# Optimization experiments

Measured on AMD Instinct MI355X. Metric: run time of the kernel, lower is better.

## Reference

```python
import jax, jax.numpy as jnp
import numpy as np

D_MODEL = 1024
N_HEADS = 16
HEAD_DIM = D_MODEL // N_HEADS
D_FF = 4 * D_MODEL
SEQ = 2048
BATCH = 2
EPS = 1e-6


def setup_inputs() -> dict:
    key = jax.random.key(0)
    ks = jax.random.split(key, 8)
    s = 0.02
    return {
        "x": jax.random.normal(ks[0], (SEQ, BATCH, D_MODEL), dtype=jnp.float32),
        "g1": jnp.ones((D_MODEL,), dtype=jnp.float32),                # norm1 weight
        "g2": jnp.ones((D_MODEL,), dtype=jnp.float32),                # norm2 weight
        "Wq": jax.random.normal(ks[1], (N_HEADS, D_MODEL, HEAD_DIM), dtype=jnp.float32) * s,
        "Wk": jax.random.normal(ks[2], (N_HEADS, D_MODEL, HEAD_DIM), dtype=jnp.float32) * s,
        "Wv": jax.random.normal(ks[3], (N_HEADS, D_MODEL, HEAD_DIM), dtype=jnp.float32) * s,
        "Wo": jax.random.normal(ks[4], (D_MODEL, D_MODEL), dtype=jnp.float32) * s,
        "W1": jax.random.normal(ks[5], (D_MODEL, D_FF), dtype=jnp.float32) * s,
        "W2": jax.random.normal(ks[6], (D_FF, D_MODEL), dtype=jnp.float32) * s,
    }


def _rmsnorm(x, g):
    rms = jnp.sqrt(jnp.mean(x * x, axis=-1, keepdims=True) + EPS)
    return g * (x / rms)


def _block(x, g1, g2, Wq, Wk, Wv, Wo, W1, W2):
    S = x.shape[0]
    scale = HEAD_DIM ** -0.5
    # --- attention (pre-norm) ---
    h = _rmsnorm(x, g1)                              # (S, B, D)
    Q = jnp.einsum('sbd,hdk->bhsk', h, Wq)           # (B, H, S, K)
    K = jnp.einsum('sbd,hdk->bhsk', h, Wk)
    V = jnp.einsum('sbd,hdk->bhsk', h, Wv)
    scores = jnp.einsum('bhsk,bhtk->bhst', Q, K) * scale
    causal = jnp.tril(jnp.ones((S, S), dtype=bool))
    scores = jnp.where(causal, scores, -jnp.inf)
    attn = jax.nn.softmax(scores, axis=-1)
    ctx = jnp.einsum('bhst,bhtk->sbhk', attn, V)     # heads concatenated in order
    ctx = ctx.reshape(S, x.shape[1], D_MODEL)
    x = x + ctx @ Wo
    # --- FFN (pre-norm) ---
    h2 = _rmsnorm(x, g2)
    x = x + jax.nn.silu(h2 @ W1) @ W2
    return x


def reference(x, g1, g2, Wq, Wk, Wv, Wo, W1, W2):
    return _block(x, g1, g2, Wq, Wk, Wv, Wo, W1, W2)
```

## Files before the change

kernel.cpp:

```cpp
#include <hip/hip_runtime.h>

typedef unsigned short u16;
typedef __bf16 bf16x8 __attribute__((ext_vector_type(8)));
typedef u16 u16x8 __attribute__((ext_vector_type(8)));
typedef u16 u16x4 __attribute__((ext_vector_type(4)));
typedef float f32x4 __attribute__((ext_vector_type(4)));

__device__ __forceinline__ u16 f2bf(float f) {
    union { float f; unsigned int u; } x; x.f = f;
    unsigned int r = x.u + 0x7FFFu + ((x.u >> 16) & 1u);
    return (u16)(r >> 16);
}

__device__ __forceinline__ u16 f2bf_hw(float f) {
    union { __bf16 b; u16 u; } x; x.b = (__bf16)f; return x.u;
}

__device__ __forceinline__ void gload_lds16(const u16* g, u16* l) {
    __builtin_amdgcn_global_load_lds(
        (const __attribute__((address_space(1))) unsigned int*)g,
        (__attribute__((address_space(3))) unsigned int*)l, 16, 0, 0);
}


__global__ __launch_bounds__(256) void qkvT_k(
    const float* __restrict__ Wq, const float* __restrict__ Wk,
    const float* __restrict__ Wv, u16* __restrict__ out)
{
    __shared__ float T[64][65];
    const int d0 = blockIdx.x * 64;
    const int y = blockIdx.y;
    const int wsel = y >> 4, h = y & 15;
    const float* W = (wsel == 0) ? Wq : (wsel == 1) ? Wk : Wv;
    const float scale = (wsel == 0) ? 0.125f * 1.44269504088896f : 1.0f;
    const int tid = threadIdx.x;
    const int tr = tid >> 4;
    const int tc = (tid & 15) * 4;
    #pragma unroll
    for (int k = 0; k < 4; k++) {
        f32x4 v = *(const f32x4*)(W + (size_t)h * 65536 + (size_t)(d0 + 16 * k + tr) * 64 + tc);
        T[16 * k + tr][tc]     = v[0];
        T[16 * k + tr][tc + 1] = v[1];
        T[16 * k + tr][tc + 2] = v[2];
        T[16 * k + tr][tc + 3] = v[3];
    }
    __syncthreads();
    #pragma unroll
    for (int k = 0; k < 4; k++) {
        const int kk = 16 * k + tr;
        u16x4 o;
        #pragma unroll
        for (int i = 0; i < 4; i++) o[i] = f2bf(T[tc + i][kk] * scale);
        *(u16x4*)(out + (size_t)(wsel * 1024 + h * 64 + kk) * 1024 + d0 + tc) = o;
    }
}

__global__ __launch_bounds__(256) void transT_k(
    const float* __restrict__ in, u16* __restrict__ out, int R, int C)
{
    __shared__ float T[64][65];
    const int r0 = blockIdx.x * 64, c0 = blockIdx.y * 64;
    const int tid = threadIdx.x;
    const int tr = tid >> 4;
    const int tc = (tid & 15) * 4;
    #pragma unroll
    for (int k = 0; k < 4; k++) {
        f32x4 v = *(const f32x4*)(in + (size_t)(c0 + 16 * k + tr) * R + r0 + tc);
        T[16 * k + tr][tc]     = v[0];
        T[16 * k + tr][tc + 1] = v[1];
        T[16 * k + tr][tc + 2] = v[2];
        T[16 * k + tr][tc + 3] = v[3];
    }
    __syncthreads();
    #pragma unroll
    for (int k = 0; k < 4; k++) {
        const int rl = 16 * k + tr;
        u16x4 o;
        #pragma unroll
        for (int i = 0; i < 4; i++) o[i] = f2bf(T[tc + i][rl]);
        *(u16x4*)(out + (size_t)(r0 + rl) * C + c0 + tc) = o;
    }
}

__global__ __launch_bounds__(256) void vtrans_k(const u16* __restrict__ qkv, u16* __restrict__ vT)
{
    __shared__ u16 T[64][72];
    const int bh = blockIdx.x, b = bh >> 4, h = bh & 15;
    const int s0 = blockIdx.y * 64;
    const int tid = threadIdx.x;
    const int r = tid >> 2, c0 = (tid & 3) * 16;
    const u16* src = qkv + ((size_t)((s0 + r) * 2 + b)) * 3072 + 2048 + h * 64 + c0;
    *(u16x8*)&T[r][c0] = *(const u16x8*)src;
    *(u16x8*)&T[r][c0 + 8] = *(const u16x8*)(src + 8);
    __syncthreads();
    u16x8 o0, o1;
    #pragma unroll
    for (int i = 0; i < 8; i++) o0[i] = T[c0 + i][r];
    #pragma unroll
    for (int i = 0; i < 8; i++) o1[i] = T[c0 + 8 + i][r];
    u16* dst = vT + (size_t)(bh * 64 + r) * 2048 + s0 + c0;
    *(u16x8*)dst = o0;
    *(u16x8*)(dst + 8) = o1;
}

__global__ __launch_bounds__(256) void rmsnorm_k(
    const float* __restrict__ x, const float* __restrict__ g, u16* __restrict__ out)
{
    const int row = blockIdx.x;
    const int tid = threadIdx.x;
    const float* xr = x + (size_t)row * 1024;
    f32x4 v = *(const f32x4*)(xr + tid * 4);
    float ss = v[0] * v[0] + v[1] * v[1] + v[2] * v[2] + v[3] * v[3];
    #pragma unroll
    for (int off = 32; off > 0; off >>= 1) ss += __shfl_down(ss, off);
    __shared__ float red[4];
    if ((tid & 63) == 0) red[tid >> 6] = ss;
    __syncthreads();
    float sum = red[0] + red[1] + red[2] + red[3];
    float rinv = rsqrtf(sum * (1.0f / 1024.0f) + 1e-6f);
    f32x4 gv = *(const f32x4*)(g + tid * 4);
    u16x4 o;
    #pragma unroll
    for (int i = 0; i < 4; i++) o[i] = f2bf(v[i] * gv[i] * rinv);
    *(u16x4*)(out + (size_t)row * 1024 + tid * 4) = o;
}

__global__ __launch_bounds__(256) void addred_norm_k(
    const float* __restrict__ res, const float* __restrict__ p0,
    const float* __restrict__ p1, const float* __restrict__ g,
    float* __restrict__ xout, u16* __restrict__ hout)
{
    const int row = blockIdx.x;
    const int tid = threadIdx.x;
    const size_t base = (size_t)row * 1024 + tid * 4;
    f32x4 a = *(const f32x4*)(res + base);
    f32x4 b = *(const f32x4*)(p0 + base);
    f32x4 c = *(const f32x4*)(p1 + base);
    f32x4 o = a + b + c;
    *(f32x4*)(xout + base) = o;
    float ss = o[0] * o[0] + o[1] * o[1] + o[2] * o[2] + o[3] * o[3];
    #pragma unroll
    for (int off = 32; off > 0; off >>= 1) ss += __shfl_down(ss, off);
    __shared__ float red[4];
    if ((tid & 63) == 0) red[tid >> 6] = ss;
    __syncthreads();
    float sum = red[0] + red[1] + red[2] + red[3];
    float rinv = rsqrtf(sum * (1.0f / 1024.0f) + 1e-6f);
    f32x4 gv = *(const f32x4*)(g + tid * 4);
    u16x4 hv;
    #pragma unroll
    for (int i = 0; i < 4; i++) hv[i] = f2bf(o[i] * gv[i] * rinv);
    *(u16x4*)(hout + base) = hv;
}

__global__ __launch_bounds__(256) void addred4_k(
    const float* __restrict__ xm, const float* __restrict__ a0,
    const float* __restrict__ a1, const float* __restrict__ a2,
    const float* __restrict__ a3, float* __restrict__ out)
{
    int i = (blockIdx.x * 256 + threadIdx.x) * 4;
    f32x4 v = *(const f32x4*)(xm + i);
    v = v + *(const f32x4*)(a0 + i);
    v = v + *(const f32x4*)(a1 + i);
    v = v + *(const f32x4*)(a2 + i);
    v = v + *(const f32x4*)(a3 + i);
    *(f32x4*)(out + i) = v;
}

template <int MODE>
__global__ __launch_bounds__(256) void gemm_bt_k(
    const u16* __restrict__ A, const u16* __restrict__ BT,
    u16* __restrict__ outB, float* __restrict__ outF, const float* __restrict__ res,
    int M, int N, int K, int klen)
{
    __shared__ u16 As[2][128 * 64];
    __shared__ u16 Bs[2][128 * 64];
    const int tid = threadIdx.x;
    const int lane = tid & 63, w = tid >> 6;
    const int wm = w >> 1, wn = w & 1;
    const int quad = lane >> 4, l15 = lane & 15;
    const int bid = blockIdx.x + gridDim.x * blockIdx.y;
    const int bj = bid >> 3;
    const int m0 = ((bid & 7) * 4 + (bj & 3)) * 128;
    const int n0 = (bj >> 2) * 128;
    const int kbeg = blockIdx.z * klen;

    f32x4 acc[4][4] = {};

    const int srow = (w << 3) + (lane >> 3);
    const int swz = ((lane & 7) ^ (lane >> 3)) << 3;
    const u16* aA = A + (size_t)(m0 + srow) * K + kbeg + swz;
    const u16* aB = BT + (size_t)(n0 + srow) * K + kbeg + swz;
    const int wo = w * 512;
    const int rsw = (l15 & 7) << 3;

    #pragma unroll
    for (int c = 0; c < 4; c++) {
        gload_lds16(aA + (size_t)(c * 32) * K, &As[0][0] + c * 2048 + wo);
        gload_lds16(aB + (size_t)(c * 32) * K, &Bs[0][0] + c * 2048 + wo);
    }

    int cur = 0;
    for (int k0 = 0; k0 < klen; k0 += 64) {
        __syncthreads();
        if (k0 + 64 < klen) {
            #pragma unroll
            for (int c = 0; c < 4; c++) {
                gload_lds16(aA + (size_t)(c * 32) * K + k0 + 64, &As[cur ^ 1][0] + c * 2048 + wo);
                gload_lds16(aB + (size_t)(c * 32) * K + k0 + 64, &Bs[cur ^ 1][0] + c * 2048 + wo);
            }
        }
        const u16* AB = &As[cur][0];
        const u16* BB = &Bs[cur][0];
        #pragma unroll
        for (int kh = 0; kh < 2; kh++) {
            const int cb = ((kh * 4 + quad) << 3);
            bf16x8 af[4], bfr[4];
            #pragma unroll
            for (int i = 0; i < 4; i++)
                af[i] = *(const bf16x8*)(AB + (wm * 64 + i * 16 + l15) * 64 + (cb ^ rsw));
            #pragma unroll
            for (int j = 0; j < 4; j++)
                bfr[j] = *(const bf16x8*)(BB + (wn * 64 + j * 16 + l15) * 64 + (cb ^ rsw));
            #pragma unroll
            for (int i = 0; i < 4; i++)
                #pragma unroll
                for (int j = 0; j < 4; j++)
                    acc[i][j] = __builtin_amdgcn_mfma_f32_16x16x32_bf16(af[i], bfr[j], acc[i][j], 0, 0, 0);
        }
        cur ^= 1;
    }

    float* outFz = (MODE == 3) ? outF + (size_t)blockIdx.z * M * N : outF;
    #pragma unroll
    for (int i = 0; i < 4; i++) {
        const int row = m0 + wm * 64 + i * 16 + quad * 4;
        #pragma unroll
        for (int j = 0; j < 4; j++) {
            const int col = n0 + wn * 64 + j * 16 + l15;
            #pragma unroll
            for (int r = 0; r < 4; r++) {
                const size_t idx = (size_t)(row + r) * N + col;
                float v = acc[i][j][r];
                if (MODE == 0) {
                    outB[idx] = f2bf_hw(v);
                } else if (MODE == 1) {
                    outF[idx] = res[idx] + v;
                } else if (MODE == 2) {
                    float e = exp2f(v * -1.44269504088896f);
                    outB[idx] = f2bf_hw(v * __builtin_amdgcn_rcpf(1.0f + e));
                } else {
                    outFz[idx] = v;
                }
            }
        }
    }
}

#define MM8(FH) \
    { _Pragma("unroll") \
      for (int i_ = 0; i_ < 4; i_++) { \
        acc[(FH)*4+i_][0] = __builtin_amdgcn_mfma_f32_16x16x32_bf16(a[i_], b0, acc[(FH)*4+i_][0], 0, 0, 0); \
        acc[(FH)*4+i_][1] = __builtin_amdgcn_mfma_f32_16x16x32_bf16(a[i_], b1, acc[(FH)*4+i_][1], 0, 0, 0); \
        acc[(FH)*4+i_][2] = __builtin_amdgcn_mfma_f32_16x16x32_bf16(a[i_], b2, acc[(FH)*4+i_][2], 0, 0, 0); \
        acc[(FH)*4+i_][3] = __builtin_amdgcn_mfma_f32_16x16x32_bf16(a[i_], b3, acc[(FH)*4+i_][3], 0, 0, 0); \
      } }

template <int MODE>
__global__ __launch_bounds__(512, 2) void gemm8p_k(
    const u16* __restrict__ A, const u16* __restrict__ BT,
    u16* __restrict__ outB, float* __restrict__ q0, float* __restrict__ q1,
    float* __restrict__ q2, float* __restrict__ q3,
    int N, int K, int klen)
{
    __shared__ u16 sm[65536];
    const int tid = threadIdx.x;
    const int lane = tid & 63, w = tid >> 6;
    const int l15 = lane & 15, quad = lane >> 4;
    const int wm = w >> 2, wn = w & 3;

    const int nwg = gridDim.x;
    const int bid = blockIdx.x;
    const int s = (bid & 7) * (nwg >> 3) + (bid >> 3);
    const int m0 = (s & 15) * 256;
    const int n0 = (s >> 4) * 256;
    const int kbeg = blockIdx.z * klen;
    const int nT = klen >> 6;

    const int srow = w * 16 + (lane >> 2);
    const int scol = (((lane & 3) ^ ((lane >> 3) & 3)) << 3);
    const u16* gA = A + (size_t)(m0 + srow) * K + kbeg + scol;
    const u16* gB = BT + (size_t)(n0 + srow) * K + kbeg + scol;
    const size_t cstep = (size_t)128 * K;

    const int rswz = ((quad ^ ((l15 >> 1) & 3)) << 3);
    const int raoff = (wm * 128 + l15) * 32 + rswz;
    const int rboff = (wn * 64 + l15) * 32 + rswz;

    f32x4 acc[8][4] = {};

    auto stA = [&](int t, int kh) {
        u16* d = sm + (t & 1) * 32768 + kh * 8192 + w * 512;
        const u16* g = gA + (size_t)(t * 64 + kh * 32);
        gload_lds16(g, d);
        gload_lds16(g + cstep, d + 4096);
    };
    auto stB = [&](int t, int kh) {
        u16* d = sm + (t & 1) * 32768 + 16384 + kh * 8192 + w * 512;
        const u16* g = gB + (size_t)(t * 64 + kh * 32);
        gload_lds16(g, d);
        gload_lds16(g + cstep, d + 4096);
    };
    bf16x8 b0, b1, b2, b3;
    auto rdB = [&](int buf, int kh) {
        const u16* p = sm + buf * 32768 + 16384 + kh * 8192 + rboff;
        b0 = *(const bf16x8*)(p);
        b1 = *(const bf16x8*)(p + 512);
        b2 = *(const bf16x8*)(p + 1024);
        b3 = *(const bf16x8*)(p + 1536);
    };
    auto rdA = [&](int buf, int kh, int fh, bf16x8* a) {
        const u16* p = sm + buf * 32768 + kh * 8192 + fh * 2048 + raoff;
        a[0] = *(const bf16x8*)(p);
        a[1] = *(const bf16x8*)(p + 512);
        a[2] = *(const bf16x8*)(p + 1024);
        a[3] = *(const bf16x8*)(p + 1536);
    };

    stA(0, 0); stB(0, 0); stA(0, 1); stB(0, 1);
    if (nT > 1) {
        stA(1, 0); stB(1, 0);
        asm volatile("s_waitcnt vmcnt(4)" ::: "memory");
    } else {
        asm volatile("s_waitcnt vmcnt(0)" ::: "memory");
    }
    __builtin_amdgcn_s_barrier();

    for (int t = 0; t < nT; t++) {
        const int buf = t & 1;
        bf16x8 a[4];
        rdA(buf, 0, 0, a); rdB(buf, 0);
        if (t + 1 < nT) stA(t + 1, 1);
        __builtin_amdgcn_s_barrier();
        asm volatile("s_waitcnt lgkmcnt(0)" ::: "memory");
        __builtin_amdgcn_sched_barrier(0);
        __builtin_amdgcn_s_setprio(1);
        MM8(0)
        __builtin_amdgcn_s_setprio(0);
        __builtin_amdgcn_s_barrier();
        rdA(buf, 0, 1, a);
        if (t + 1 < nT) stB(t + 1, 1);
        __builtin_amdgcn_s_barrier();
        asm volatile("s_waitcnt lgkmcnt(0)" ::: "memory");
        __builtin_amdgcn_sched_barrier(0);
        __builtin_amdgcn_s_setprio(1);
        MM8(1)
        __builtin_amdgcn_s_setprio(0);
        __builtin_amdgcn_s_barrier();
        rdA(buf, 1, 0, a); rdB(buf, 1);
        if (t + 2 < nT) stA(t + 2, 0);
        __builtin_amdgcn_s_barrier();
        asm volatile("s_waitcnt lgkmcnt(0)" ::: "memory");
        __builtin_amdgcn_sched_barrier(0);
        __builtin_amdgcn_s_setprio(1);
        MM8(0)
        __builtin_amdgcn_s_setprio(0);
        __builtin_amdgcn_s_barrier();
        rdA(buf, 1, 1, a);
        if (t + 2 < nT) {
            stB(t + 2, 0);
            asm volatile("s_waitcnt vmcnt(4)" ::: "memory");
        } else {
            asm volatile("s_waitcnt vmcnt(0)" ::: "memory");
        }
        __builtin_amdgcn_s_barrier();
        asm volatile("s_waitcnt lgkmcnt(0)" ::: "memory");
        __builtin_amdgcn_sched_barrier(0);
        __builtin_amdgcn_s_setprio(1);
        MM8(1)
        __builtin_amdgcn_s_setprio(0);
        __builtin_amdgcn_s_barrier();
    }

    float* po = nullptr;
    if (MODE == 3)
        po = (blockIdx.z == 0) ? q0 : (blockIdx.z == 1) ? q1 : (blockIdx.z == 2) ? q2 : q3;
    #pragma unroll
    for (int mf = 0; mf < 8; mf++) {
        const int row = m0 + wm * 128 + mf * 16 + quad * 4;
        #pragma unroll
        for (int nf = 0; nf < 4; nf++) {
            const int col = n0 + wn * 64 + nf * 16 + l15;
            #pragma unroll
            for (int r = 0; r < 4; r++) {
                const size_t idx = (size_t)(row + r) * N + col;
                const float v = acc[mf][nf][r];
                if (MODE == 0) {
                    outB[idx] = f2bf_hw(v);
                } else if (MODE == 2) {
                    float e = exp2f(v * -1.44269504088896f);
                    outB[idx] = f2bf_hw(v * __builtin_amdgcn_rcpf(1.0f + e));
                } else {
                    po[idx] = v;
                }
            }
        }
    }
}

__global__ __launch_bounds__(256, 4) void attn_k(const u16* __restrict__ qkv,
                                                 const u16* __restrict__ vT,
                                                 u16* __restrict__ ctx)
{
    const int bh = blockIdx.x;
    const int qt = 31 - (int)blockIdx.y;
    const int b = bh >> 4, h = bh & 15;
    const int q0 = qt * 64;
    const int tid = threadIdx.x;
    const int lane = tid & 63, w = tid >> 6;
    const int quad = lane >> 4, l15 = lane & 15;

    __shared__ u16 Ks[2][4096];
    __shared__ u16 Vs[2][4096];

    const int q = q0 + 16 * w + l15;
    const u16* qrow = qkv + ((size_t)(q * 2 + b)) * 3072 + h * 64;
    const bf16x8 aq0 = *(const bf16x8*)(qrow + quad * 8);
    const bf16x8 aq1 = *(const bf16x8*)(qrow + 32 + quad * 8);

    bf16x8 ones;
    #pragma unroll
    for (int i = 0; i < 8; i++) ones[i] = (__bf16)1.0f;

    const int kr = (w << 3) + (lane >> 3);
    const int swz = ((lane & 7) ^ (lane >> 3)) << 3;
    const int ldsoff = w * 512;
    const u16* kbase0 = qkv + ((size_t)(kr * 2 + b)) * 3072 + 1024 + h * 64 + swz;
    const u16* kbase1 = kbase0 + (size_t)32 * 2 * 3072;
    const u16* vrow0 = vT + (size_t)(bh * 64 + kr) * 2048 + swz;
    const u16* vrow1 = vrow0 + (size_t)32 * 2048;

    const int sl = (l15 & 3) | ((l15 & 4) << 1) | ((l15 & 8) >> 1);
    const int rswk = (sl & 7) << 3;
    const int rswv = (l15 & 7) << 3;
    const int sq = ((quad & 1) << 1) | (quad >> 1);
    const int qloc = 16 * w + l15;

    f32x4 o[4] = {};
    f32x4 accl = {};

    gload_lds16(kbase0, &Ks[0][0] + ldsoff);
    gload_lds16(kbase1, &Ks[0][0] + 2048 + ldsoff);
    gload_lds16(vrow0, &Vs[0][0] + ldsoff);
    gload_lds16(vrow1, &Vs[0][0] + 2048 + ldsoff);

    int cur = 0;
    for (int t0 = 0; t0 <= q0; t0 += 64) {
        __syncthreads();
        if (t0 + 64 <= q0) {
            const size_t go = (size_t)(t0 + 64) * 2 * 3072;
            u16* KB = &Ks[cur ^ 1][0];
            u16* VB = &Vs[cur ^ 1][0];
            gload_lds16(kbase0 + go, KB + ldsoff);
            gload_lds16(kbase1 + go, KB + 2048 + ldsoff);
            gload_lds16(vrow0 + (t0 + 64), VB + ldsoff);
            gload_lds16(vrow1 + (t0 + 64), VB + 2048 + ldsoff);
        }
        const u16* KB = &Ks[cur][0];
        const u16* VB = &Vs[cur][0];

        f32x4 s[4];
        __builtin_amdgcn_s_setprio(1);
        #pragma unroll
        for (int tg = 0; tg < 4; tg++) {
            const u16* kb = KB + (16 * tg + sl) * 64;
            bf16x8 ak0 = *(const bf16x8*)(kb + ((quad << 3) ^ rswk));
            bf16x8 ak1 = *(const bf16x8*)(kb + (((quad + 4) << 3) ^ rswk));
            f32x4 c = {};
            c = __builtin_amdgcn_mfma_f32_16x16x32_bf16(ak0, aq0, c, 0, 0, 0);
            c = __builtin_amdgcn_mfma_f32_16x16x32_bf16(ak1, aq1, c, 0, 0, 0);
            s[tg] = c;
        }
        __builtin_amdgcn_s_setprio(0);

        if (t0 == q0) {
            #pragma unroll
            for (int tg = 0; tg < 4; tg++)
                #pragma unroll
                for (int r = 0; r < 4; r++)
                    if ((16 * tg + 4 * sq + r) > qloc) s[tg][r] = -1e30f;
        }

        unsigned dd[4][2];
        #pragma unroll
        for (int tg = 0; tg < 4; tg++) {
            float e0 = exp2f(s[tg][0]), e1 = exp2f(s[tg][1]);
            float e2 = exp2f(s[tg][2]), e3 = exp2f(s[tg][3]);
            asm("v_cvt_pk_bf16_f32 %0, %1, %2" : "=v"(dd[tg][0]) : "v"(e0), "v"(e1));
            asm("v_cvt_pk_bf16_f32 %0, %1, %2" : "=v"(dd[tg][1]) : "v"(e2), "v"(e3));
        }
        unsigned x0 = dd[0][0], y0 = dd[1][0];
        asm volatile("v_permlane32_swap_b32 %0, %1" : "+v"(x0), "+v"(y0));
        unsigned x1 = dd[0][1], y1 = dd[1][1];
        asm volatile("v_permlane32_swap_b32 %0, %1" : "+v"(x1), "+v"(y1));
        unsigned x2 = dd[2][0], y2 = dd[3][0];
        asm volatile("v_permlane32_swap_b32 %0, %1" : "+v"(x2), "+v"(y2));
        unsigned x3 = dd[2][1], y3 = dd[3][1];
        asm volatile("v_permlane32_swap_b32 %0, %1" : "+v"(x3), "+v"(y3));

        union { unsigned u[4]; bf16x8 v; } pu0, pu1;
        pu0.u[0] = x0; pu0.u[1] = x1; pu0.u[2] = y0; pu0.u[3] = y1;
        pu1.u[0] = x2; pu1.u[1] = x3; pu1.u[2] = y2; pu1.u[3] = y3;
        const bf16x8 pf0 = pu0.v, pf1 = pu1.v;

        __builtin_amdgcn_s_setprio(1);
        accl = __builtin_amdgcn_mfma_f32_16x16x32_bf16(ones, pf0, accl, 0, 0, 0);
        accl = __builtin_amdgcn_mfma_f32_16x16x32_bf16(ones, pf1, accl, 0, 0, 0);
        #pragma unroll
        for (int i = 0; i < 4; i++) {
            const u16* vb = VB + (i * 16 + l15) * 64;
            bf16x8 av0 = *(const bf16x8*)(vb + ((quad << 3) ^ rswv));
            bf16x8 av1 = *(const bf16x8*)(vb + (((quad + 4) << 3) ^ rswv));
            o[i] = __builtin_amdgcn_mfma_f32_16x16x32_bf16(av0, pf0, o[i], 0, 0, 0);
            o[i] = __builtin_amdgcn_mfma_f32_16x16x32_bf16(av1, pf1, o[i], 0, 0, 0);
        }
        __builtin_amdgcn_s_setprio(0);
        cur ^= 1;
    }

    const float linv = 1.0f / accl[0];
    #pragma unroll
    for (int i = 0; i < 4; i++) {
        u16x4 ov;
        #pragma unroll
        for (int r = 0; r < 4; r++) ov[r] = f2bf_hw(o[i][r] * linv);
        *(u16x4*)(ctx + ((size_t)(q * 2 + b)) * 1024 + h * 64 + i * 16 + quad * 4) = ov;
    }
}

extern "C" void kernel_launch(void* const* d_in, const int* in_sizes, int n_in,
                              void* d_out, int out_size, void* d_ws, size_t ws_size,
                              hipStream_t stream)
{
    (void)in_sizes; (void)n_in; (void)out_size; (void)ws_size;
    const float* x  = (const float*)d_in[0];
    const float* g1 = (const float*)d_in[1];
    const float* g2 = (const float*)d_in[2];
    const float* Wq = (const float*)d_in[3];
    const float* Wk = (const float*)d_in[4];
    const float* Wv = (const float*)d_in[5];
    const float* Wo = (const float*)d_in[6];
    const float* W1 = (const float*)d_in[7];
    const float* W2 = (const float*)d_in[8];
    float* out = (float*)d_out;

    char* ws = (char*)d_ws;
    u16*   bqkvT = (u16*)(ws);
    u16*   woT   = (u16*)(ws + 6291456);
    u16*   w1T   = (u16*)(ws + 8388608);
    u16*   w2T   = (u16*)(ws + 16777216);
    u16*   h1    = (u16*)(ws + 25165824);
    u16*   qkvB  = (u16*)(ws + 33554432);
    u16*   vT    = (u16*)(ws + 25165824);
    u16*   ctxB  = (u16*)(ws + 58720256);
    float* xmid  = (float*)(ws + 41943040);
    u16*   h2    = (u16*)(ws + 83886080);
    u16*   actB  = (u16*)(ws + 92274688);
    float* partO = (float*)(ws + 92274688);
    float* p0 = (float*)(ws);
    float* p1 = (float*)(ws + 25165824);
    float* p2 = (float*)(ws + 58720256);
    float* p3 = (float*)(ws + 75497472);

    qkvT_k<<<dim3(16, 48), 256, 0, stream>>>(Wq, Wk, Wv, bqkvT);
    transT_k<<<dim3(16, 16), 256, 0, stream>>>(Wo, woT, 1024, 1024);
    transT_k<<<dim3(64, 16), 256, 0, stream>>>(W1, w1T, 4096, 1024);
    transT_k<<<dim3(16, 64), 256, 0, stream>>>(W2, w2T, 1024, 4096);

    rmsnorm_k<<<4096, 256, 0, stream>>>(x, g1, h1);

    gemm8p_k<0><<<dim3(192, 1, 1), 512, 0, stream>>>(h1, bqkvT, qkvB,
                                                     nullptr, nullptr, nullptr, nullptr,
                                                     3072, 1024, 1024);
    vtrans_k<<<dim3(32, 32), 256, 0, stream>>>(qkvB, vT);
    attn_k<<<dim3(32, 32), 256, 0, stream>>>(qkvB, vT, ctxB);

    gemm_bt_k<3><<<dim3(8, 32, 2), 256, 0, stream>>>(ctxB, woT, nullptr, partO, nullptr,
                                                     4096, 1024, 1024, 512);
    addred_norm_k<<<4096, 256, 0, stream>>>(x, partO, partO + 4096 * 1024, g2, xmid, h2);

    gemm8p_k<2><<<dim3(256, 1, 1), 512, 0, stream>>>(h2, w1T, actB,
                                                     nullptr, nullptr, nullptr, nullptr,
                                                     4096, 1024, 1024);
    gemm8p_k<3><<<dim3(64, 1, 4), 512, 0, stream>>>(actB, w2T, nullptr,
                                                    p0, p1, p2, p3,
                                                    1024, 4096, 1024);
    addred4_k<<<4096 * 1024 / 1024, 256, 0, stream>>>(xmid, p0, p1, p2, p3, out);
}
```

Measured before the change: 321.0 us.

## Fuse V transpose into QKV GEMM epilogue and double-buffer LDS fragment reads

The QKV GEMM gains a mode whose epilogue writes the V columns directly in transposed layout for attention, which removes the separate vtrans kernel and its extra read and write of V. The gemm8p main loop now uses two register sets for A and B fragments, so LDS reads for the next MFMA group are issued before the current group runs. This hides LDS latency behind MFMA work. The cost is more registers per thread and narrow strided stores for V in the epilogue.

```diff
diff --git a/kernel.cpp b/kernel.cpp
--- a/kernel.cpp
+++ b/kernel.cpp
@@ -80,27 +80,6 @@
         for (int i = 0; i < 4; i++) o[i] = f2bf(T[tc + i][rl]);
         *(u16x4*)(out + (size_t)(r0 + rl) * C + c0 + tc) = o;
     }
-}
-
-__global__ __launch_bounds__(256) void vtrans_k(const u16* __restrict__ qkv, u16* __restrict__ vT)
-{
-    __shared__ u16 T[64][72];
-    const int bh = blockIdx.x, b = bh >> 4, h = bh & 15;
-    const int s0 = blockIdx.y * 64;
-    const int tid = threadIdx.x;
-    const int r = tid >> 2, c0 = (tid & 3) * 16;
-    const u16* src = qkv + ((size_t)((s0 + r) * 2 + b)) * 3072 + 2048 + h * 64 + c0;
-    *(u16x8*)&T[r][c0] = *(const u16x8*)src;
-    *(u16x8*)&T[r][c0 + 8] = *(const u16x8*)(src + 8);
-    __syncthreads();
-    u16x8 o0, o1;
-    #pragma unroll
-    for (int i = 0; i < 8; i++) o0[i] = T[c0 + i][r];
-    #pragma unroll
-    for (int i = 0; i < 8; i++) o1[i] = T[c0 + 8 + i][r];
-    u16* dst = vT + (size_t)(bh * 64 + r) * 2048 + s0 + c0;
-    *(u16x8*)dst = o0;
-    *(u16x8*)(dst + 8) = o1;
 }
 
 __global__ __launch_bounds__(256) void rmsnorm_k(
@@ -257,20 +236,23 @@
     }
 }
 
-#define MM8(FH) \
+#define MMQ(FH, AS, BS) \
     { _Pragma("unroll") \
       for (int i_ = 0; i_ < 4; i_++) { \
-        acc[(FH)*4+i_][0] = __builtin_amdgcn_mfma_f32_16x16x32_bf16(a[i_], b0, acc[(FH)*4+i_][0], 0, 0, 0); \
-        acc[(FH)*4+i_][1] = __builtin_amdgcn_mfma_f32_16x16x32_bf16(a[i_], b1, acc[(FH)*4+i_][1], 0, 0, 0); \
-        acc[(FH)*4+i_][2] = __builtin_amdgcn_mfma_f32_16x16x32_bf16(a[i_], b2, acc[(FH)*4+i_][2], 0, 0, 0); \
-        acc[(FH)*4+i_][3] = __builtin_amdgcn_mfma_f32_16x16x32_bf16(a[i_], b3, acc[(FH)*4+i_][3], 0, 0, 0); \
+        acc[(FH)*4+i_][0] = __builtin_amdgcn_mfma_f32_16x16x32_bf16(AS[i_], BS[0], acc[(FH)*4+i_][0], 0, 0, 0); \
+        acc[(FH)*4+i_][1] = __builtin_amdgcn_mfma_f32_16x16x32_bf16(AS[i_], BS[1], acc[(FH)*4+i_][1], 0, 0, 0); \
+        acc[(FH)*4+i_][2] = __builtin_amdgcn_mfma_f32_16x16x32_bf16(AS[i_], BS[2], acc[(FH)*4+i_][2], 0, 0, 0); \
+        acc[(FH)*4+i_][3] = __builtin_amdgcn_mfma_f32_16x16x32_bf16(AS[i_], BS[3], acc[(FH)*4+i_][3], 0, 0, 0); \
       } }
+
+#define LGKM0  asm volatile("s_waitcnt lgkmcnt(0)" ::: "memory"); __builtin_amdgcn_sched_barrier(0)
+#define SBAR   __builtin_amdgcn_s_barrier()
 
 template <int MODE>
 __global__ __launch_bounds__(512, 2) void gemm8p_k(
     const u16* __restrict__ A, const u16* __restrict__ BT,
     u16* __restrict__ outB, float* __restrict__ q0, float* __restrict__ q1,
-    float* __restrict__ q2, float* __restrict__ q3,
+    float* __restrict__ q2, float* __restrict__ q3, u16* __restrict__ vTout,
     int N, int K, int klen)
 {
     __shared__ u16 sm[65536];
@@ -311,13 +293,12 @@
         gload_lds16(g, d);
         gload_lds16(g + cstep, d + 4096);
     };
-    bf16x8 b0, b1, b2, b3;
-    auto rdB = [&](int buf, int kh) {
+    auto rdB = [&](int buf, int kh, bf16x8* b) {
         const u16* p = sm + buf * 32768 + 16384 + kh * 8192 + rboff;
-        b0 = *(const bf16x8*)(p);
-        b1 = *(const bf16x8*)(p + 512);
-        b2 = *(const bf16x8*)(p + 1024);
-        b3 = *(const bf16x8*)(p + 1536);
+        b[0] = *(const bf16x8*)(p);
+        b[1] = *(const bf16x8*)(p + 512);
+        b[2] = *(const bf16x8*)(p + 1024);
+        b[3] = *(const bf16x8*)(p + 1536);
     };
     auto rdA = [&](int buf, int kh, int fh, bf16x8* a) {
         const u16* p = sm + buf * 32768 + kh * 8192 + fh * 2048 + raoff;
@@ -327,6 +308,8 @@
         a[3] = *(const bf16x8*)(p + 1536);
     };
 
+    bf16x8 aX[4], aY[4], bX[4], bY[4];
+
     stA(0, 0); stB(0, 0); stA(0, 1); stB(0, 1);
     if (nT > 1) {
         stA(1, 0); stB(1, 0);
@@ -334,74 +317,93 @@
     } else {
         asm volatile("s_waitcnt vmcnt(0)" ::: "memory");
     }
-    __builtin_amdgcn_s_barrier();
+    SBAR;
+    rdA(0, 0, 0, aX); rdB(0, 0, bX);
 
     for (int t = 0; t < nT; t++) {
-        const int buf = t & 1;
-        bf16x8 a[4];
-        rdA(buf, 0, 0, a); rdB(buf, 0);
+        const int buf = t & 1, nbuf = buf ^ 1;
         if (t + 1 < nT) stA(t + 1, 1);
-        __builtin_amdgcn_s_barrier();
-        asm volatile("s_waitcnt lgkmcnt(0)" ::: "memory");
+        SBAR;
+        LGKM0;
+        rdA(buf, 0, 1, aY);
         __builtin_amdgcn_sched_barrier(0);
         __builtin_amdgcn_s_setprio(1);
-        MM8(0)
+        MMQ(0, aX, bX)
         __builtin_amdgcn_s_setprio(0);
-        __builtin_amdgcn_s_barrier();
-        rdA(buf, 0, 1, a);
+        SBAR;
         if (t + 1 < nT) stB(t + 1, 1);
-        __builtin_amdgcn_s_barrier();
-        asm volatile("s_waitcnt lgkmcnt(0)" ::: "memory");
+        SBAR;
+        LGKM0;
+        rdA(buf, 1, 0, aX); rdB(buf, 1, bY);
         __builtin_amdgcn_sched_barrier(0);
         __builtin_amdgcn_s_setprio(1);
-        MM8(1)
+        MMQ(1, aY, bX)
         __builtin_amdgcn_s_setprio(0);
-        __builtin_amdgcn_s_barrier();
-        rdA(buf, 1, 0, a); rdB(buf, 1);
+        SBAR;
         if (t + 2 < nT) stA(t + 2, 0);
-        __builtin_amdgcn_s_barrier();
-        asm volatile("s_waitcnt lgkmcnt(0)" ::: "memory");
+        SBAR;
+        LGKM0;
+        rdA(buf, 1, 1, aY);
         __builtin_amdgcn_sched_barrier(0);
         __builtin_amdgcn_s_setprio(1);
-        MM8(0)
+        MMQ(0, aX, bY)
         __builtin_amdgcn_s_setprio(0);
-        __builtin_amdgcn_s_barrier();
-        rdA(buf, 1, 1, a);
+        SBAR;
         if (t + 2 < nT) {
             stB(t + 2, 0);
             asm volatile("s_waitcnt vmcnt(4)" ::: "memory");
         } else {
             asm volatile("s_waitcnt vmcnt(0)" ::: "memory");
         }
-        __builtin_amdgcn_s_barrier();
-        asm volatile("s_waitcnt lgkmcnt(0)" ::: "memory");
+        SBAR;
+        LGKM0;
+        if (t + 1 < nT) { rdA(nbuf, 0, 0, aX); rdB(nbuf, 0, bX); }
         __builtin_amdgcn_sched_barrier(0);
         __builtin_amdgcn_s_setprio(1);
-        MM8(1)
+        MMQ(1, aY, bY)
         __builtin_amdgcn_s_setprio(0);
-        __builtin_amdgcn_s_barrier();
+        SBAR;
     }
 
     float* po = nullptr;
     if (MODE == 3)
         po = (blockIdx.z == 0) ? q0 : (blockIdx.z == 1) ? q1 : (blockIdx.z == 2) ? q2 : q3;
-    #pragma unroll
-    for (int mf = 0; mf < 8; mf++) {
-        const int row = m0 + wm * 128 + mf * 16 + quad * 4;
-        #pragma unroll
-        for (int nf = 0; nf < 4; nf++) {
-            const int col = n0 + wn * 64 + nf * 16 + l15;
-            #pragma unroll
-            for (int r = 0; r < 4; r++) {
-                const size_t idx = (size_t)(row + r) * N + col;
-                const float v = acc[mf][nf][r];
-                if (MODE == 0) {
-                    outB[idx] = f2bf_hw(v);
-                } else if (MODE == 2) {
-                    float e = exp2f(v * -1.44269504088896f);
-                    outB[idx] = f2bf_hw(v * __builtin_amdgcn_rcpf(1.0f + e));
-                } else {
-                    po[idx] = v;
+
+    if (MODE == 4 && n0 >= 2048) {
+        #pragma unroll
+        for (int mf = 0; mf < 8; mf++) {
+            const int row = m0 + wm * 128 + mf * 16 + quad * 4;
+            const int s0 = row >> 1;
+            #pragma unroll
+            for (int nf = 0; nf < 4; nf++) {
+                const int cv = n0 + wn * 64 + nf * 16 + l15 - 2048;
+                const int h = cv >> 6, d = cv & 63;
+                const f32x4 v = acc[mf][nf];
+                unsigned p0v = (unsigned)f2bf_hw(v[0]) | ((unsigned)f2bf_hw(v[2]) << 16);
+                unsigned p1v = (unsigned)f2bf_hw(v[1]) | ((unsigned)f2bf_hw(v[3]) << 16);
+                *(unsigned*)(vTout + ((size_t)(h * 64 + d) * 2048 + s0)) = p0v;
+                *(unsigned*)(vTout + ((size_t)((16 + h) * 64 + d) * 2048 + s0)) = p1v;
+            }
+        }
+    } else {
+        #pragma unroll
+        for (int mf = 0; mf < 8; mf++) {
+            const int row = m0 + wm * 128 + mf * 16 + quad * 4;
+            #pragma unroll
+            for (int nf = 0; nf < 4; nf++) {
+                const int col = n0 + wn * 64 + nf * 16 + l15;
+                #pragma unroll
+                for (int r = 0; r < 4; r++) {
+                    const size_t idx = (size_t)(row + r) * N + col;
+                    const float v = acc[mf][nf][r];
+                    if (MODE == 0 || MODE == 4) {
+                        outB[idx] = f2bf_hw(v);
+                    } else if (MODE == 2) {
+                        float e = exp2f(v * -1.44269504088896f);
+                        outB[idx] = f2bf_hw(v * __builtin_amdgcn_rcpf(1.0f + e));
+                    } else {
+                        po[idx] = v;
+                    }
                 }
             }
         }
@@ -561,7 +563,7 @@
     u16*   w2T   = (u16*)(ws + 16777216);
     u16*   h1    = (u16*)(ws + 25165824);
     u16*   qkvB  = (u16*)(ws + 33554432);
-    u16*   vT    = (u16*)(ws + 25165824);
+    u16*   vT2   = (u16*)(ws + 75497472);
     u16*   ctxB  = (u16*)(ws + 58720256);
     float* xmid  = (float*)(ws + 41943040);
     u16*   h2    = (u16*)(ws + 83886080);
@@ -579,11 +581,10 @@
 
     rmsnorm_k<<<4096, 256, 0, stream>>>(x, g1, h1);
 
-    gemm8p_k<0><<<dim3(192, 1, 1), 512, 0, stream>>>(h1, bqkvT, qkvB,
+    gemm8p_k<4><<<dim3(192, 1, 1), 512, 0, stream>>>(h1, bqkvT, qkvB,
                                                      nullptr, nullptr, nullptr, nullptr,
-                                                     3072, 1024, 1024);
-    vtrans_k<<<dim3(32, 32), 256, 0, stream>>>(qkvB, vT);
-    attn_k<<<dim3(32, 32), 256, 0, stream>>>(qkvB, vT, ctxB);
+                                                     vT2, 3072, 1024, 1024);
+    attn_k<<<dim3(32, 32), 256, 0, stream>>>(qkvB, vT2, ctxB);
 
     gemm_bt_k<3><<<dim3(8, 32, 2), 256, 0, stream>>>(ctxB, woT, nullptr, partO, nullptr,
                                                      4096, 1024, 1024, 512);
@@ -591,9 +592,9 @@
 
     gemm8p_k<2><<<dim3(256, 1, 1), 512, 0, stream>>>(h2, w1T, actB,
                                                      nullptr, nullptr, nullptr, nullptr,
-                                                     4096, 1024, 1024);
+                                                     nullptr, 4096, 1024, 1024);
     gemm8p_k<3><<<dim3(64, 1, 4), 512, 0, stream>>>(actB, w2T, nullptr,
                                                     p0, p1, p2, p3,
-                                                    1024, 4096, 1024);
+                                                    nullptr, 1024, 4096, 1024);
     addred4_k<<<4096 * 1024 / 1024, 256, 0, stream>>>(xmid, p0, p1, p2, p3, out);
 }
```

Result: slower. 329.8 us (+2.7%).

## Fuse weight-prep kernels and first RMSNorm into one launch; relax GEMM barrier waits

Applied to the files above, without the earlier changes.

Merges the QKV weight transpose, the three other weight transposes and the first RMSNorm into a single prep kernel dispatched by block index, removing four launches and the gaps between them. Separately, the gemm8p main loop drops the explicit lgkmcnt(0) waits and sched_barriers before each MFMA group and uses only s_barrier plus a compiler memory fence. It also passes B fragments as an array. This lets the compiler schedule LDS reads and MFMAs itself. It relies on the compiler inserting the correct LDS waits, and the new ordering may be worse than the hand-tuned one.

```diff
diff --git a/kernel.cpp b/kernel.cpp
--- a/kernel.cpp
+++ b/kernel.cpp
@@ -23,44 +23,11 @@
 }
 
 
-__global__ __launch_bounds__(256) void qkvT_k(
-    const float* __restrict__ Wq, const float* __restrict__ Wk,
-    const float* __restrict__ Wv, u16* __restrict__ out)
-{
-    __shared__ float T[64][65];
-    const int d0 = blockIdx.x * 64;
-    const int y = blockIdx.y;
-    const int wsel = y >> 4, h = y & 15;
-    const float* W = (wsel == 0) ? Wq : (wsel == 1) ? Wk : Wv;
-    const float scale = (wsel == 0) ? 0.125f * 1.44269504088896f : 1.0f;
-    const int tid = threadIdx.x;
-    const int tr = tid >> 4;
-    const int tc = (tid & 15) * 4;
-    #pragma unroll
-    for (int k = 0; k < 4; k++) {
-        f32x4 v = *(const f32x4*)(W + (size_t)h * 65536 + (size_t)(d0 + 16 * k + tr) * 64 + tc);
-        T[16 * k + tr][tc]     = v[0];
-        T[16 * k + tr][tc + 1] = v[1];
-        T[16 * k + tr][tc + 2] = v[2];
-        T[16 * k + tr][tc + 3] = v[3];
-    }
-    __syncthreads();
-    #pragma unroll
-    for (int k = 0; k < 4; k++) {
-        const int kk = 16 * k + tr;
-        u16x4 o;
-        #pragma unroll
-        for (int i = 0; i < 4; i++) o[i] = f2bf(T[tc + i][kk] * scale);
-        *(u16x4*)(out + (size_t)(wsel * 1024 + h * 64 + kk) * 1024 + d0 + tc) = o;
-    }
-}
-
-__global__ __launch_bounds__(256) void transT_k(
-    const float* __restrict__ in, u16* __restrict__ out, int R, int C)
-{
-    __shared__ float T[64][65];
-    const int r0 = blockIdx.x * 64, c0 = blockIdx.y * 64;
-    const int tid = threadIdx.x;
+__device__ __forceinline__ void transT_body(
+    const float* __restrict__ in, u16* __restrict__ out, int R, int C,
+    int bx, int by, float T[64][65], int tid)
+{
+    const int r0 = bx * 64, c0 = by * 64;
     const int tr = tid >> 4;
     const int tc = (tid & 15) * 4;
     #pragma unroll
@@ -79,6 +46,72 @@
         #pragma unroll
         for (int i = 0; i < 4; i++) o[i] = f2bf(T[tc + i][rl]);
         *(u16x4*)(out + (size_t)(r0 + rl) * C + c0 + tc) = o;
+    }
+}
+
+__global__ __launch_bounds__(256) void prep_k(
+    const float* __restrict__ Wq, const float* __restrict__ Wk,
+    const float* __restrict__ Wv, const float* __restrict__ Wo,
+    const float* __restrict__ W1, const float* __restrict__ W2,
+    const float* __restrict__ x, const float* __restrict__ g1,
+    u16* __restrict__ bqkvT, u16* __restrict__ woT,
+    u16* __restrict__ w1T, u16* __restrict__ w2T, u16* __restrict__ h1)
+{
+    __shared__ float T[64][65];
+    const int id = blockIdx.x;
+    const int tid = threadIdx.x;
+
+    if (id < 768) {
+        const int bx = id & 15, y = id >> 4;
+        const int d0 = bx * 64;
+        const int wsel = y >> 4, h = y & 15;
+        const float* W = (wsel == 0) ? Wq : (wsel == 1) ? Wk : Wv;
+        const float scale = (wsel == 0) ? 0.125f * 1.44269504088896f : 1.0f;
+        const int tr = tid >> 4;
+        const int tc = (tid & 15) * 4;
+        #pragma unroll
+        for (int k = 0; k < 4; k++) {
+            f32x4 v = *(const f32x4*)(W + (size_t)h * 65536 + (size_t)(d0 + 16 * k + tr) * 64 + tc);
+            T[16 * k + tr][tc]     = v[0];
+            T[16 * k + tr][tc + 1] = v[1];
+            T[16 * k + tr][tc + 2] = v[2];
+            T[16 * k + tr][tc + 3] = v[3];
+        }
+        __syncthreads();
+        #pragma unroll
+        for (int k = 0; k < 4; k++) {
+            const int kk = 16 * k + tr;
+            u16x4 o;
+            #pragma unroll
+            for (int i = 0; i < 4; i++) o[i] = f2bf(T[tc + i][kk] * scale);
+            *(u16x4*)(bqkvT + (size_t)(wsel * 1024 + h * 64 + kk) * 1024 + d0 + tc) = o;
+        }
+    } else if (id < 1024) {
+        const int id2 = id - 768;
+        transT_body(Wo, woT, 1024, 1024, id2 & 15, id2 >> 4, T, tid);
+    } else if (id < 2048) {
+        const int id3 = id - 1024;
+        transT_body(W1, w1T, 4096, 1024, id3 & 63, id3 >> 6, T, tid);
+    } else if (id < 3072) {
+        const int id4 = id - 2048;
+        transT_body(W2, w2T, 1024, 4096, id4 & 15, id4 >> 4, T, tid);
+    } else {
+        const int row = id - 3072;
+        const float* xr = x + (size_t)row * 1024;
+        f32x4 v = *(const f32x4*)(xr + tid * 4);
+        float ss = v[0] * v[0] + v[1] * v[1] + v[2] * v[2] + v[3] * v[3];
+        #pragma unroll
+        for (int off = 32; off > 0; off >>= 1) ss += __shfl_down(ss, off);
+        float* red = &T[0][0];
+        if ((tid & 63) == 0) red[tid >> 6] = ss;
+        __syncthreads();
+        float sum = red[0] + red[1] + red[2] + red[3];
+        float rinv = rsqrtf(sum * (1.0f / 1024.0f) + 1e-6f);
+        f32x4 gv = *(const f32x4*)(g1 + tid * 4);
+        u16x4 o;
+        #pragma unroll
+        for (int i = 0; i < 4; i++) o[i] = f2bf(v[i] * gv[i] * rinv);
+        *(u16x4*)(h1 + (size_t)row * 1024 + tid * 4) = o;
     }
 }
 
@@ -101,28 +134,6 @@
     u16* dst = vT + (size_t)(bh * 64 + r) * 2048 + s0 + c0;
     *(u16x8*)dst = o0;
     *(u16x8*)(dst + 8) = o1;
-}
-
-__global__ __launch_bounds__(256) void rmsnorm_k(
-    const float* __restrict__ x, const float* __restrict__ g, u16* __restrict__ out)
-{
-    const int row = blockIdx.x;
-    const int tid = threadIdx.x;
-    const float* xr = x + (size_t)row * 1024;
-    f32x4 v = *(const f32x4*)(xr + tid * 4);
-    float ss = v[0] * v[0] + v[1] * v[1] + v[2] * v[2] + v[3] * v[3];
-    #pragma unroll
-    for (int off = 32; off > 0; off >>= 1) ss += __shfl_down(ss, off);
-    __shared__ float red[4];
-    if ((tid & 63) == 0) red[tid >> 6] = ss;
-    __syncthreads();
-    float sum = red[0] + red[1] + red[2] + red[3];
-    float rinv = rsqrtf(sum * (1.0f / 1024.0f) + 1e-6f);
-    f32x4 gv = *(const f32x4*)(g + tid * 4);
-    u16x4 o;
-    #pragma unroll
-    for (int i = 0; i < 4; i++) o[i] = f2bf(v[i] * gv[i] * rinv);
-    *(u16x4*)(out + (size_t)row * 1024 + tid * 4) = o;
 }
 
 __global__ __launch_bounds__(256) void addred_norm_k(
@@ -257,14 +268,17 @@
     }
 }
 
-#define MM8(FH) \
+#define MMQ(FH, AS, BS) \
     { _Pragma("unroll") \
       for (int i_ = 0; i_ < 4; i_++) { \
-        acc[(FH)*4+i_][0] = __builtin_amdgcn_mfma_f32_16x16x32_bf16(a[i_], b0, acc[(FH)*4+i_][0], 0, 0, 0); \
-        acc[(FH)*4+i_][1] = __builtin_amdgcn_mfma_f32_16x16x32_bf16(a[i_], b1, acc[(FH)*4+i_][1], 0, 0, 0); \
-        acc[(FH)*4+i_][2] = __builtin_amdgcn_mfma_f32_16x16x32_bf16(a[i_], b2, acc[(FH)*4+i_][2], 0, 0, 0); \
-        acc[(FH)*4+i_][3] = __builtin_amdgcn_mfma_f32_16x16x32_bf16(a[i_], b3, acc[(FH)*4+i_][3], 0, 0, 0); \
+        acc[(FH)*4+i_][0] = __builtin_amdgcn_mfma_f32_16x16x32_bf16(AS[i_], BS[0], acc[(FH)*4+i_][0], 0, 0, 0); \
+        acc[(FH)*4+i_][1] = __builtin_amdgcn_mfma_f32_16x16x32_bf16(AS[i_], BS[1], acc[(FH)*4+i_][1], 0, 0, 0); \
+        acc[(FH)*4+i_][2] = __builtin_amdgcn_mfma_f32_16x16x32_bf16(AS[i_], BS[2], acc[(FH)*4+i_][2], 0, 0, 0); \
+        acc[(FH)*4+i_][3] = __builtin_amdgcn_mfma_f32_16x16x32_bf16(AS[i_], BS[3], acc[(FH)*4+i_][3], 0, 0, 0); \
       } }
+
+#define SBAR   __builtin_amdgcn_s_barrier()
+#define FENCE  asm volatile("" ::: "memory")
 
 template <int MODE>
 __global__ __launch_bounds__(512, 2) void gemm8p_k(
@@ -311,13 +325,12 @@
         gload_lds16(g, d);
         gload_lds16(g + cstep, d + 4096);
     };
-    bf16x8 b0, b1, b2, b3;
-    auto rdB = [&](int buf, int kh) {
+    auto rdB = [&](int buf, int kh, bf16x8* b) {
         const u16* p = sm + buf * 32768 + 16384 + kh * 8192 + rboff;
-        b0 = *(const bf16x8*)(p);
-        b1 = *(const bf16x8*)(p + 512);
-        b2 = *(const bf16x8*)(p + 1024);
-        b3 = *(const bf16x8*)(p + 1536);
+        b[0] = *(const bf16x8*)(p);
+        b[1] = *(const bf16x8*)(p + 512);
+        b[2] = *(const bf16x8*)(p + 1024);
+        b[3] = *(const bf16x8*)(p + 1536);
     };
     auto rdA = [&](int buf, int kh, int fh, bf16x8* a) {
         const u16* p = sm + buf * 32768 + kh * 8192 + fh * 2048 + raoff;
@@ -334,38 +347,32 @@
     } else {
         asm volatile("s_waitcnt vmcnt(0)" ::: "memory");
     }
-    __builtin_amdgcn_s_barrier();
+    SBAR; FENCE;
 
     for (int t = 0; t < nT; t++) {
         const int buf = t & 1;
-        bf16x8 a[4];
-        rdA(buf, 0, 0, a); rdB(buf, 0);
+        bf16x8 a[4], b[4];
+        rdA(buf, 0, 0, a); rdB(buf, 0, b);
         if (t + 1 < nT) stA(t + 1, 1);
-        __builtin_amdgcn_s_barrier();
-        asm volatile("s_waitcnt lgkmcnt(0)" ::: "memory");
-        __builtin_amdgcn_sched_barrier(0);
+        SBAR; FENCE;
         __builtin_amdgcn_s_setprio(1);
-        MM8(0)
+        MMQ(0, a, b)
         __builtin_amdgcn_s_setprio(0);
-        __builtin_amdgcn_s_barrier();
+        SBAR; FENCE;
         rdA(buf, 0, 1, a);
         if (t + 1 < nT) stB(t + 1, 1);
-        __builtin_amdgcn_s_barrier();
-        asm volatile("s_waitcnt lgkmcnt(0)" ::: "memory");
-        __builtin_amdgcn_sched_barrier(0);
+        SBAR; FENCE;
         __builtin_amdgcn_s_setprio(1);
-        MM8(1)
+        MMQ(1, a, b)
         __builtin_amdgcn_s_setprio(0);
-        __builtin_amdgcn_s_barrier();
-        rdA(buf, 1, 0, a); rdB(buf, 1);
+        SBAR; FENCE;
+        rdA(buf, 1, 0, a); rdB(buf, 1, b);
         if (t + 2 < nT) stA(t + 2, 0);
-        __builtin_amdgcn_s_barrier();
-        asm volatile("s_waitcnt lgkmcnt(0)" ::: "memory");
-        __builtin_amdgcn_sched_barrier(0);
+        SBAR; FENCE;
         __builtin_amdgcn_s_setprio(1);
-        MM8(0)
+        MMQ(0, a, b)
         __builtin_amdgcn_s_setprio(0);
-        __builtin_amdgcn_s_barrier();
+        SBAR; FENCE;
         rdA(buf, 1, 1, a);
         if (t + 2 < nT) {
             stB(t + 2, 0);
@@ -373,13 +380,11 @@
         } else {
             asm volatile("s_waitcnt vmcnt(0)" ::: "memory");
         }
-        __builtin_amdgcn_s_barrier();
-        asm volatile("s_waitcnt lgkmcnt(0)" ::: "memory");
-        __builtin_amdgcn_sched_barrier(0);
+        SBAR; FENCE;
         __builtin_amdgcn_s_setprio(1);
-        MM8(1)
+        MMQ(1, a, b)
         __builtin_amdgcn_s_setprio(0);
-        __builtin_amdgcn_s_barrier();
+        SBAR; FENCE;
     }
 
     float* po = nullptr;
@@ -572,12 +577,8 @@
     float* p2 = (float*)(ws + 58720256);
     float* p3 = (float*)(ws + 75497472);
 
-    qkvT_k<<<dim3(16, 48), 256, 0, stream>>>(Wq, Wk, Wv, bqkvT);
-    transT_k<<<dim3(16, 16), 256, 0, stream>>>(Wo, woT, 1024, 1024);
-    transT_k<<<dim3(64, 16), 256, 0, stream>>>(W1, w1T, 4096, 1024);
-    transT_k<<<dim3(16, 64), 256, 0, stream>>>(W2, w2T, 1024, 4096);
-
-    rmsnorm_k<<<4096, 256, 0, stream>>>(x, g1, h1);
+    prep_k<<<7168, 256, 0, stream>>>(Wq, Wk, Wv, Wo, W1, W2, x, g1,
+                                     bqkvT, woT, w1T, w2T, h1);
 
     gemm8p_k<0><<<dim3(192, 1, 1), 512, 0, stream>>>(h1, bqkvT, qkvB,
                                                      nullptr, nullptr, nullptr, nullptr,
```

Measured after the change: 312.2 us. 2.8% less time.
